# Kernel tuning notes

Measured on AMD Instinct MI355X. Metric: run time of the kernel, lower is better.

## Reference

```python
import jax, jax.numpy as jnp
import numpy as np

K = 20  # neighbors
SLOPE = 0.2  # leaky relu negative slope


def knn_idx(x):
    # x: [B, C, N] -> idx: [B, N, K] indices of K nearest points (incl. self)
    inner = -2.0 * jnp.einsum('bcn,bcm->bnm', x, x)          # [B,N,N]
    xx = jnp.sum(x * x, axis=1)                              # [B,N]
    pairwise = -xx[:, :, None] - inner - xx[:, None, :]      # negative sq dist
    _, idx = jax.lax.top_k(pairwise, K)                      # [B,N,K]
    return idx


def graph_feature(x, idx):
    # x: [B, C, N], idx: [B, N, K] -> [B, N, K, 2C] = cat(neighbor - center, center)
    xt = jnp.transpose(x, (0, 2, 1))                         # [B,N,C]
    nbr = jnp.take_along_axis(xt[:, None, :, :], idx[..., None], axis=2)  # [B,N,K,C]
    ctr = jnp.broadcast_to(xt[:, :, None, :], nbr.shape)     # [B,N,K,C]
    return jnp.concatenate([nbr - ctr, ctr], axis=-1)        # [B,N,K,2C]


def edge_block(x, W):
    # x: [B, C, N]; W: [C_out, 2C] (1x1 conv weight, no bias)
    f = graph_feature(x, knn_idx(x))                         # [B,N,K,2C]
    y = jnp.einsum('bnkc,oc->bonk', f, W)                    # [B,C_out,N,K]
    y = jax.nn.leaky_relu(y, negative_slope=SLOPE)
    return jnp.max(y, axis=-1)                               # [B,C_out,N]


def setup_inputs() -> dict:
    key = jax.random.key(0)
    ks = jax.random.split(key, 6)
    B, N = 8, 2048
    x = jax.random.normal(ks[0], (B, 3, N), dtype=jnp.float32)
    def w(k, o, i):
        return jax.random.normal(k, (o, i), dtype=jnp.float32) * (1.0 / np.sqrt(i))
    W1 = w(ks[1], 64, 6)      # block1: in 3  -> 64
    W2 = w(ks[2], 64, 128)    # block2: in 64 -> 64
    W3 = w(ks[3], 128, 128)   # block3: in 64 -> 128
    W4 = w(ks[4], 256, 256)   # block4: in 128-> 256
    Wg = w(ks[5], 1024, 512)  # global conv1d: 64+64+128+256=512 -> 1024
    return {'x': x, 'W1': W1, 'W2': W2, 'W3': W3, 'W4': W4, 'Wg': Wg}


def reference(x, W1, W2, W3, W4, Wg):
    x1 = edge_block(x, W1)                                   # [B,64,N]
    x2 = edge_block(x1, W2)                                  # [B,64,N]
    x3 = edge_block(x2, W3)                                  # [B,128,N]
    x4 = edge_block(x3, W4)                                  # [B,256,N]
    x_cat = jnp.concatenate([x1, x2, x3, x4], axis=1)        # [B,512,N]
    g = jnp.einsum('bcn,oc->bon', x_cat, Wg)                 # [B,1024,N]
    g = jax.nn.leaky_relu(g, negative_slope=SLOPE)
    return jnp.max(g, axis=-1)                               # [B,1024]
```

## Files before the change

kernel.cpp:

```cpp
#include <hip/hip_runtime.h>
#include <hip/hip_bf16.h>
#include <cfloat>

#define Nn 2048
#define KK 20
#define BB 8
#define SLOPE 0.2f
#define NCH 32

typedef __bf16 bf16x8 __attribute__((ext_vector_type(8)));
typedef float f32x4 __attribute__((ext_vector_type(4)));
typedef unsigned short u16x8 __attribute__((ext_vector_type(8)));

__device__ __forceinline__ unsigned short bfbits(__hip_bfloat16 h) {
    unsigned short us;
    __builtin_memcpy(&us, &h, 2);
    return us;
}


__global__ void wfrag_kernel(const float* __restrict__ W,
                             __hip_bfloat16* __restrict__ Wh, __hip_bfloat16* __restrict__ Wl,
                             int CIN, int Co, int CO2, int KS) {
    int g = blockIdx.x * 256 + threadIdx.x;
    int ng = CO2 * KS * 4;
    if (g >= ng) return;
    int o = g / (KS * 4);
    int c8 = (g - o * (KS * 4)) * 8;
    u16x8 hw, lw;
    #pragma unroll
    for (int t = 0; t < 8; ++t) {
        int c = c8 + t;
        float v = 0.f;
        if (c < CIN) {
            if (o < Co) v = W[(long)o * 2 * CIN + c];
            else        v = W[(long)(o - Co) * 2 * CIN + CIN + c] - W[(long)(o - Co) * 2 * CIN + c];
        }
        __hip_bfloat16 h = __float2bfloat16(v);
        hw[t] = bfbits(h);
        lw[t] = bfbits(__float2bfloat16(v - __bfloat162float(h)));
    }
    long dst = ((long)(o >> 4) * KS + (c8 >> 5)) * 512 + ((o & 15) + 16 * ((c8 >> 3) & 3)) * 8;
    *(u16x8*)(Wh + dst) = hw;
    *(u16x8*)(Wl + dst) = lw;
}

__global__ void tobf16_frag(const float* __restrict__ W, __hip_bfloat16* __restrict__ F) {
    int g = blockIdx.x * 256 + threadIdx.x;
    if (g >= 1024 * 64) return;
    int o = g >> 6, k8 = (g & 63) * 8;
    const float* src = W + (long)o * 512 + k8;
    unsigned short tmp[8];
    #pragma unroll
    for (int t = 0; t < 8; ++t) tmp[t] = bfbits(__float2bfloat16(src[t]));
    long dst = ((long)(o >> 4) * 16 + (k8 >> 5)) * 512 + ((o & 15) + 16 * ((k8 >> 3) & 3)) * 8;
    u16x8 pk;
    #pragma unroll
    for (int t = 0; t < 8; ++t) pk[t] = tmp[t];
    *(u16x8*)(F + dst) = pk;
}

__global__ void split3_kernel(const float* __restrict__ x,
                              __hip_bfloat16* __restrict__ xh,
                              __hip_bfloat16* __restrict__ xl,
                              float* __restrict__ sq) {
    int i = blockIdx.x * 256 + threadIdx.x;
    if (i >= BB * Nn) return;
    const float* xb = x + (long)(i >> 11) * 3 * Nn + (i & 2047);
    float v0 = xb[0], v1 = xb[Nn], v2 = xb[2 * Nn];
    sq[i] = v0 * v0 + v1 * v1 + v2 * v2;
    __hip_bfloat16 h0 = __float2bfloat16(v0), h1 = __float2bfloat16(v1), h2 = __float2bfloat16(v2);
    __hip_bfloat16 l0 = __float2bfloat16(v0 - __bfloat162float(h0));
    __hip_bfloat16 l1 = __float2bfloat16(v1 - __bfloat162float(h1));
    __hip_bfloat16 l2 = __float2bfloat16(v2 - __bfloat162float(h2));
    long base = ((long)(i >> 11) * 128 + ((i & 2047) >> 4)) * 512 + (long)(i & 15) * 8;
    u16x8 z = (u16x8){0, 0, 0, 0, 0, 0, 0, 0};
    u16x8 hw = z, lw = z;
    hw[0] = bfbits(h0); hw[1] = bfbits(h1); hw[2] = bfbits(h2);
    lw[0] = bfbits(l0); lw[1] = bfbits(l1); lw[2] = bfbits(l2);
    *(u16x8*)(xh + base) = hw;
    *(u16x8*)(xl + base) = lw;
    #pragma unroll
    for (int q = 1; q < 4; ++q) {
        *(u16x8*)(xh + base + q * 128) = z;
        *(u16x8*)(xl + base + q * 128) = z;
    }
}

__device__ __forceinline__ unsigned fkey(float f) {
    unsigned u = __float_as_uint(f);
    return u ^ (((unsigned)((int)u >> 31)) | 0x80000000u);
}

template<int C, int NKS>
__global__ void __launch_bounds__(512)
gram_mfma(const __hip_bfloat16* __restrict__ xh, const __hip_bfloat16* __restrict__ xl,
          int ks0, const float* __restrict__ sqv, unsigned* __restrict__ Kbuf) {
    constexpr int KS = C / 32;
    const int tid = threadIdx.x;
    const int w = tid >> 6, lane = tid & 63;
    const int lm = lane & 15, quad = lane >> 4;
    const int nb = blockIdx.x & 7;
    const int mt = (blockIdx.x >> 3) & 15;
    const int b  = blockIdx.x >> 7;
    const int m0 = mt * 128 + (w >> 2) * 64;
    const int j0 = nb * 256 + (w & 3) * 64;

    const long TILE = (long)NKS * 512;
    const __hip_bfloat16* hbase = xh + (long)b * 128 * TILE + (long)ks0 * 512 + lane * 8;
    const __hip_bfloat16* lbase = xl + (long)b * 128 * TILE + (long)ks0 * 512 + lane * 8;
    const __hip_bfloat16* hA = hbase + (long)(m0 >> 4) * TILE;
    const __hip_bfloat16* lA = lbase + (long)(m0 >> 4) * TILE;
    const __hip_bfloat16* hB = hbase + (long)(j0 >> 4) * TILE;
    const __hip_bfloat16* lB = lbase + (long)(j0 >> 4) * TILE;

    f32x4 acc[4][4];
    #pragma unroll
    for (int i = 0; i < 4; ++i)
        #pragma unroll
        for (int j = 0; j < 4; ++j)
            acc[i][j] = (f32x4){0.f, 0.f, 0.f, 0.f};

    #pragma unroll 2
    for (int ks = 0; ks < KS; ++ks) {
        bf16x8 ah[4], alo[4], bh[4], blo[4];
        #pragma unroll
        for (int i = 0; i < 4; ++i) {
            ah[i]  = *(const bf16x8*)(const void*)(hA + (long)i * TILE + ks * 512);
            alo[i] = *(const bf16x8*)(const void*)(lA + (long)i * TILE + ks * 512);
        }
        #pragma unroll
        for (int j = 0; j < 4; ++j) {
            bh[j]  = *(const bf16x8*)(const void*)(hB + (long)j * TILE + ks * 512);
            blo[j] = *(const bf16x8*)(const void*)(lB + (long)j * TILE + ks * 512);
        }
        #pragma unroll
        for (int i = 0; i < 4; ++i)
            #pragma unroll
            for (int j = 0; j < 4; ++j) {
                acc[i][j] = __builtin_amdgcn_mfma_f32_16x16x32_bf16(alo[i], bh[j], acc[i][j], 0, 0, 0);
                acc[i][j] = __builtin_amdgcn_mfma_f32_16x16x32_bf16(ah[i], blo[j], acc[i][j], 0, 0, 0);
                acc[i][j] = __builtin_amdgcn_mfma_f32_16x16x32_bf16(ah[i], bh[j], acc[i][j], 0, 0, 0);
            }
    }

    const float* sqb = sqv + b * Nn;
    float sqj[4];
    #pragma unroll
    for (int j = 0; j < 4; ++j) sqj[j] = sqb[j0 + j * 16 + lm];

    unsigned* Kb = Kbuf + (long)b * Nn * Nn;
    #pragma unroll
    for (int i = 0; i < 4; ++i) {
        #pragma unroll
        for (int r = 0; r < 4; ++r) {
            int m = m0 + i * 16 + quad * 4 + r;
            unsigned* row = Kb + (long)m * Nn;
            #pragma unroll
            for (int j = 0; j < 4; ++j)
                row[j0 + j * 16 + lm] = fkey(fmaf(-2.f, acc[i][j][r], sqj[j]));
        }
    }
}

template<int KS, int NKS_A, int CO2>
__global__ void __launch_bounds__(256)
proj_mfma(const __hip_bfloat16* __restrict__ Ah, const __hip_bfloat16* __restrict__ Al,
          int ks0,
          const __hip_bfloat16* __restrict__ Wh, const __hip_bfloat16* __restrict__ Wl,
          float* __restrict__ Z) {
    constexpr int NWo = (CO2 >= 256) ? 4 : 2;
    constexpr int NWm = 4 / NWo;
    constexpr int MT = 2048 / (64 * NWm);
    const int tid = threadIdx.x;
    const int w = tid >> 6, lane = tid & 63;
    const int lm = lane & 15, quad = lane >> 4;
    const int b  = blockIdx.x & 7;
    const int mt = (blockIdx.x >> 3) % MT;
    const int ot = (blockIdx.x >> 3) / MT;
    const int m0 = mt * 64 * NWm + (w / NWo) * 64;
    const int o0 = ot * 64 * NWo + (w % NWo) * 64;

    const long TA = (long)NKS_A * 512;
    const long TW = (long)KS * 512;
    const __hip_bfloat16* hA = Ah + (long)b * 128 * TA + (long)(m0 >> 4) * TA + (long)ks0 * 512 + lane * 8;
    const __hip_bfloat16* lA = Al + (long)b * 128 * TA + (long)(m0 >> 4) * TA + (long)ks0 * 512 + lane * 8;
    const __hip_bfloat16* hW = Wh + (long)(o0 >> 4) * TW + lane * 8;
    const __hip_bfloat16* lW = Wl + (long)(o0 >> 4) * TW + lane * 8;

    f32x4 acc[4][4];
    #pragma unroll
    for (int i = 0; i < 4; ++i)
        #pragma unroll
        for (int j = 0; j < 4; ++j)
            acc[i][j] = (f32x4){0.f, 0.f, 0.f, 0.f};

    #pragma unroll 2
    for (int ks = 0; ks < KS; ++ks) {
        bf16x8 ah[4], alo[4], bh[4], blo[4];
        #pragma unroll
        for (int i = 0; i < 4; ++i) {
            ah[i]  = *(const bf16x8*)(const void*)(hA + (long)i * TA + ks * 512);
            alo[i] = *(const bf16x8*)(const void*)(lA + (long)i * TA + ks * 512);
        }
        #pragma unroll
        for (int j = 0; j < 4; ++j) {
            bh[j]  = *(const bf16x8*)(const void*)(hW + (long)j * TW + ks * 512);
            blo[j] = *(const bf16x8*)(const void*)(lW + (long)j * TW + ks * 512);
        }
        #pragma unroll
        for (int i = 0; i < 4; ++i)
            #pragma unroll
            for (int j = 0; j < 4; ++j) {
                acc[i][j] = __builtin_amdgcn_mfma_f32_16x16x32_bf16(alo[i], bh[j], acc[i][j], 0, 0, 0);
                acc[i][j] = __builtin_amdgcn_mfma_f32_16x16x32_bf16(ah[i], blo[j], acc[i][j], 0, 0, 0);
                acc[i][j] = __builtin_amdgcn_mfma_f32_16x16x32_bf16(ah[i], bh[j], acc[i][j], 0, 0, 0);
            }
    }

    float* Zb = Z + (long)b * 2048 * CO2;
    #pragma unroll
    for (int i = 0; i < 4; ++i) {
        #pragma unroll
        for (int r = 0; r < 4; ++r) {
            int n = m0 + i * 16 + quad * 4 + r;
            float* row = Zb + (long)n * CO2 + o0;
            #pragma unroll
            for (int j = 0; j < 4; ++j)
                row[j * 16 + lm] = acc[i][j][r];
        }
    }
}

__global__ void __launch_bounds__(512)
select_kernel(const unsigned* __restrict__ Kbuf, int* __restrict__ idx) {
    const int tid = threadIdx.x;
    const int b  = blockIdx.x >> 8;
    const int n0 = (blockIdx.x & 255) * 8;
    const int w = tid >> 6, lane = tid & 63;

    const unsigned* drow = Kbuf + ((long)b * Nn + n0 + w) * Nn;
    int* outp = idx + ((long)b * Nn + n0 + w) * KK;

    unsigned long long lm1 = ~0ull, lm2 = ~0ull;
    #pragma unroll
    for (int jj = 0; jj < 8; ++jj) {
        int j4 = (jj * 64 + lane) * 4;
        uint4 v = *(const uint4*)(drow + j4);
        unsigned long long kk0 = ((unsigned long long)v.x << 32) | (unsigned)(j4 + 0);
        unsigned long long kk1 = ((unsigned long long)v.y << 32) | (unsigned)(j4 + 1);
        unsigned long long kk2 = ((unsigned long long)v.z << 32) | (unsigned)(j4 + 2);
        unsigned long long kk3 = ((unsigned long long)v.w << 32) | (unsigned)(j4 + 3);
        unsigned long long hi;
        hi = kk0 > lm1 ? kk0 : lm1; lm1 = kk0 < lm1 ? kk0 : lm1; lm2 = hi < lm2 ? hi : lm2;
        hi = kk1 > lm1 ? kk1 : lm1; lm1 = kk1 < lm1 ? kk1 : lm1; lm2 = hi < lm2 ? hi : lm2;
        hi = kk2 > lm1 ? kk2 : lm1; lm1 = kk2 < lm1 ? kk2 : lm1; lm2 = hi < lm2 ? hi : lm2;
        hi = kk3 > lm1 ? kk3 : lm1; lm1 = kk3 < lm1 ? kk3 : lm1; lm2 = hi < lm2 ? hi : lm2;
    }

    unsigned T;
    {
        unsigned sa = (unsigned)(lm1 >> 32), sb = (unsigned)(lm2 >> 32);
        #pragma unroll
        for (int size = 2; size <= 128; size <<= 1) {
            #pragma unroll
            for (int str = size >> 1; str >= 2; str >>= 1) {
                const int h = str >> 1;
                const bool asc = (((lane << 1) & size) == 0);
                const bool keepmin = (((lane & h) == 0) == asc);
                unsigned pa = __shfl_xor(sa, h, 64);
                unsigned pb = __shfl_xor(sb, h, 64);
                sa = keepmin ? (sa < pa ? sa : pa) : (sa > pa ? sa : pa);
                sb = keepmin ? (sb < pb ? sb : pb) : (sb > pb ? sb : pb);
            }
            const bool asc = (((lane << 1) & size) == 0);
            unsigned mn = sa < sb ? sa : sb;
            unsigned mx = sa < sb ? sb : sa;
            sa = asc ? mn : mx; sb = asc ? mx : mn;
        }
        T = __shfl(sb, 9, 64);
    }

    unsigned long long c0 = 0, c1 = 0, c2 = 0, c3 = 0, c4 = 0, c5 = 0;
    unsigned cnt = 0;
    #pragma unroll
    for (int jj = 0; jj < 8; ++jj) {
        int j4 = (jj * 64 + lane) * 4;
        uint4 v = *(const uint4*)(drow + j4);
        #pragma unroll
        for (int q = 0; q < 4; ++q) {
            unsigned kq = q == 0 ? v.x : q == 1 ? v.y : q == 2 ? v.z : v.w;
            if (kq <= T) {
                unsigned long long kv = ((unsigned long long)kq << 32) | (unsigned)(j4 + q);
                if (cnt == 0) c0 = kv;
                else if (cnt == 1) c1 = kv;
                else if (cnt == 2) c2 = kv;
                else if (cnt == 3) c3 = kv;
                else if (cnt == 4) c4 = kv;
                else if (cnt == 5) c5 = kv;
                ++cnt;
            }
        }
    }

    unsigned tot = cnt;
    #pragma unroll
    for (int s = 1; s < 64; s <<= 1) tot += __shfl_xor(tot, s, 64);
    unsigned long long anyovf = __ballot(cnt > 6);

    if (anyovf == 0 && tot <= 56) {
        int e = (int)tot - KK;
        for (int rr = 0; rr < e; ++rr) {
            unsigned long long mymax = c0;
            if (c1 > mymax) mymax = c1;
            if (c2 > mymax) mymax = c2;
            if (c3 > mymax) mymax = c3;
            if (c4 > mymax) mymax = c4;
            if (c5 > mymax) mymax = c5;
            unsigned long long wm = mymax;
            #pragma unroll
            for (int s = 1; s < 64; s <<= 1) {
                unsigned long long o = __shfl_xor(wm, s, 64);
                wm = o > wm ? o : wm;
            }
            if (mymax == wm) {
                if (c5 == wm) c5 = 0;
                else if (c4 == wm) c4 = 0;
                else if (c3 == wm) c3 = 0;
                else if (c2 == wm) c2 = 0;
                else if (c1 == wm) c1 = 0;
                else c0 = 0;
            }
        }
        unsigned myc = (c0 != 0) + (c1 != 0) + (c2 != 0) + (c3 != 0) + (c4 != 0) + (c5 != 0);
        unsigned inc = myc;
        #pragma unroll
        for (int off = 1; off < 64; off <<= 1) {
            unsigned t2 = __shfl_up(inc, off, 64);
            if (lane >= off) inc += t2;
        }
        int p = (int)(inc - myc);
        if (c0 != 0) outp[p++] = (int)(unsigned)c0;
        if (c1 != 0) outp[p++] = (int)(unsigned)c1;
        if (c2 != 0) outp[p++] = (int)(unsigned)c2;
        if (c3 != 0) outp[p++] = (int)(unsigned)c3;
        if (c4 != 0) outp[p++] = (int)(unsigned)c4;
        if (c5 != 0) outp[p++] = (int)(unsigned)c5;
        return;
    }

    unsigned exl[KK];
    int ne = 0;
    auto scan2x = [&](unsigned long long& m1, unsigned long long& m2) {
        m1 = ~0ull; m2 = ~0ull;
        for (int jj = 0; jj < 8; ++jj) {
            int j4 = (jj * 64 + lane) * 4;
            uint4 v = *(const uint4*)(drow + j4);
            #pragma unroll
            for (int q = 0; q < 4; ++q) {
                unsigned kq = q == 0 ? v.x : q == 1 ? v.y : q == 2 ? v.z : v.w;
                for (int t = 0; t < ne; ++t)
                    if (exl[t] == (unsigned)(j4 + q)) kq = 0xFFFFFFFFu;
                unsigned long long kv = ((unsigned long long)kq << 32) | (unsigned)(j4 + q);
                unsigned long long hi = kv > m1 ? kv : m1;
                m1 = kv < m1 ? kv : m1;
                m2 = hi < m2 ? hi : m2;
            }
        }
    };

    for (int k = 0; k < KK; ++k) {
        unsigned key = (unsigned)(lm1 >> 32);
        unsigned bk = key;
        #pragma unroll
        for (int s = 1; s < 64; s <<= 1) {
            unsigned ob = __shfl_xor(bk, s, 64);
            bk = ob < bk ? ob : bk;
        }
        unsigned long long winners = __ballot(key == bk);
        int wl = (int)(__ffsll((unsigned long long)winners) - 1);
        int bi = (int)__shfl((unsigned)lm1, wl, 64);
        if (lane == 0) outp[k] = bi;
        if (lane == wl) {
            exl[ne++] = (unsigned)bi;
            if (lm2 != ~0ull) { lm1 = lm2; lm2 = ~0ull; }
            else scan2x(lm1, lm2);
        }
    }
}

template<int CO, bool EMIT>
__global__ void __launch_bounds__(256)
gather_max(const float* __restrict__ Z, const int* __restrict__ idx,
           __hip_bfloat16* __restrict__ xbT, __hip_bfloat16* __restrict__ xbTlo,
           float* __restrict__ sqv, int coff) {
    constexpr int CO2 = 2 * CO;
    constexpr int VEC = CO / 64;
    __shared__ int ji[16][KK];
    const int tid = threadIdx.x;
    const int b  = blockIdx.x & 7;
    const int n0 = (blockIdx.x >> 3) * 16;
    const float* Zb = Z + (long)b * 2048 * CO2;

    for (int t = tid; t < 16 * KK; t += 256) {
        int nn = t / KK, k = t - nn * KK;
        ji[nn][k] = idx[((long)b * Nn + n0 + nn) * KK + k];
    }
    __syncthreads();

    const int w = tid >> 6, lane = tid & 63;
    for (int i = 0; i < 4; ++i) {
        int nl = w * 4 + i, n = n0 + nl;
        float mx[VEC];
        #pragma unroll
        for (int v = 0; v < VEC; ++v) mx[v] = -FLT_MAX;
        for (int k = 0; k < KK; ++k) {
            int m = ji[nl][k];
            const float* zr = Zb + (long)m * CO2 + lane * VEC;
            if constexpr (VEC == 4) {
                float4 zv = *(const float4*)zr;
                mx[0] = fmaxf(mx[0], zv.x); mx[1] = fmaxf(mx[1], zv.y);
                mx[2] = fmaxf(mx[2], zv.z); mx[3] = fmaxf(mx[3], zv.w);
            } else if constexpr (VEC == 2) {
                float2 zv = *(const float2*)zr;
                mx[0] = fmaxf(mx[0], zv.x); mx[1] = fmaxf(mx[1], zv.y);
            } else {
                mx[0] = fmaxf(mx[0], zr[0]);
            }
        }
        const float* zc = Zb + (long)n * CO2 + CO + lane * VEC;
        const int c0 = coff + lane * VEC;
        const long fbase = ((long)b * 128 + (n >> 4)) * 8192
                         + (long)(c0 >> 5) * 512
                         + (long)(((n & 15) + 16 * ((c0 >> 3) & 3)) * 8) + (c0 & 7);
        __hip_bfloat16* xr = xbT + fbase;
        float y[VEC];
        if constexpr (VEC == 4) {
            float4 cv = *(const float4*)zc;
            y[0] = mx[0] + cv.x; y[1] = mx[1] + cv.y; y[2] = mx[2] + cv.z; y[3] = mx[3] + cv.w;
        } else if constexpr (VEC == 2) {
            float2 cv = *(const float2*)zc;
            y[0] = mx[0] + cv.x; y[1] = mx[1] + cv.y;
        } else {
            y[0] = mx[0] + zc[0];
        }
        unsigned short hb[VEC], lb[VEC];
        float s = 0.f;
        #pragma unroll
        for (int v = 0; v < VEC; ++v) {
            y[v] = y[v] > 0.f ? y[v] : SLOPE * y[v];
            __hip_bfloat16 h = __float2bfloat16(y[v]);
            hb[v] = bfbits(h);
            if constexpr (EMIT) {
                lb[v] = bfbits(__float2bfloat16(y[v] - __bfloat162float(h)));
                s += y[v] * y[v];
            }
        }
        if constexpr (VEC == 4) {
            ushort4 pk; pk.x = hb[0]; pk.y = hb[1]; pk.z = hb[2]; pk.w = hb[3];
            *(ushort4*)xr = pk;
        } else if constexpr (VEC == 2) {
            ushort2 pk; pk.x = hb[0]; pk.y = hb[1];
            *(ushort2*)xr = pk;
        } else {
            *(unsigned short*)xr = hb[0];
        }
        if constexpr (EMIT) {
            __hip_bfloat16* lr = xbTlo + fbase;
            if constexpr (VEC == 4) {
                ushort4 pk; pk.x = lb[0]; pk.y = lb[1]; pk.z = lb[2]; pk.w = lb[3];
                *(ushort4*)lr = pk;
            } else if constexpr (VEC == 2) {
                ushort2 pk; pk.x = lb[0]; pk.y = lb[1];
                *(ushort2*)lr = pk;
            } else {
                *(unsigned short*)lr = lb[0];
            }
            #pragma unroll
            for (int off = 1; off < 64; off <<= 1) s += __shfl_xor(s, off, 64);
            if (lane == 0) sqv[b * Nn + n] = s;
        }
    }
}

__global__ void __launch_bounds__(512)
global_mfma(const __hip_bfloat16* __restrict__ Wgf,
            const __hip_bfloat16* __restrict__ xbT,
            float* __restrict__ partial) {
    const int tid = threadIdx.x;
    const int w = tid >> 6, lane = tid & 63;
    const int lm = lane & 15, quad = lane >> 4;
    const int b  = blockIdx.x >> 6;
    const int ot = (blockIdx.x >> 3) & 7;
    const int nb = blockIdx.x & 7;
    const int o0 = ot * 128 + (w >> 2) * 64;
    const int nbw = nb * 256 + (w & 3) * 64;

    const __hip_bfloat16* Af = Wgf + (long)(o0 >> 4) * 8192 + lane * 8;
    const __hip_bfloat16* Bf = xbT + ((long)b * 128 + (nbw >> 4)) * 8192 + lane * 8;

    f32x4 acc[4][4];
    #pragma unroll
    for (int mt = 0; mt < 4; ++mt)
        #pragma unroll
        for (int nt = 0; nt < 4; ++nt)
            acc[mt][nt] = (f32x4){0.f, 0.f, 0.f, 0.f};

    #pragma unroll 2
    for (int ks = 0; ks < 16; ++ks) {
        bf16x8 a[4], bb[4];
        #pragma unroll
        for (int mt = 0; mt < 4; ++mt)
            a[mt] = *(const bf16x8*)(const void*)(Af + (long)mt * 8192 + ks * 512);
        #pragma unroll
        for (int nt = 0; nt < 4; ++nt)
            bb[nt] = *(const bf16x8*)(const void*)(Bf + (long)nt * 8192 + ks * 512);
        #pragma unroll
        for (int mt = 0; mt < 4; ++mt)
            #pragma unroll
            for (int nt = 0; nt < 4; ++nt)
                acc[mt][nt] = __builtin_amdgcn_mfma_f32_16x16x32_bf16(
                    a[mt], bb[nt], acc[mt][nt], 0, 0, 0);
    }

    #pragma unroll
    for (int mt = 0; mt < 4; ++mt) {
        #pragma unroll
        for (int r = 0; r < 4; ++r) {
            float v = fmaxf(fmaxf(acc[mt][0][r], acc[mt][1][r]),
                            fmaxf(acc[mt][2][r], acc[mt][3][r]));
            #pragma unroll
            for (int s = 1; s < 16; s <<= 1)
                v = fmaxf(v, __shfl_xor(v, s, 16));
            if (lm == 0) {
                int o = o0 + mt * 16 + quad * 4 + r;
                partial[((long)b * 1024 + o) * NCH + nb * 4 + (w & 3)] = v;
            }
        }
    }
}

__global__ void gmax_kernel(const float* __restrict__ partial, float* __restrict__ out) {
    int i = blockIdx.x * 256 + threadIdx.x;
    float m = -FLT_MAX;
    #pragma unroll
    for (int j = 0; j < NCH; ++j) m = fmaxf(m, partial[(long)i * NCH + j]);
    out[i] = m > 0.f ? m : SLOPE * m;
}

extern "C" void kernel_launch(void* const* d_in, const int* in_sizes, int n_in,
                              void* d_out, int out_size, void* d_ws, size_t ws_size,
                              hipStream_t stream) {
    const float* x  = (const float*)d_in[0];
    const float* W1 = (const float*)d_in[1];
    const float* W2 = (const float*)d_in[2];
    const float* W3 = (const float*)d_in[3];
    const float* W4 = (const float*)d_in[4];
    const float* Wg = (const float*)d_in[5];
    float* out = (float*)d_out;

    int*   idxb = (int*)d_ws;
    float* part = (float*)(idxb + (long)BB * Nn * KK);
    __hip_bfloat16* Wgb = (__hip_bfloat16*)(part + (long)BB * 1024 * NCH);
    __hip_bfloat16* xbT = Wgb + (long)1024 * 512;
    __hip_bfloat16* xbTlo = xbT + (long)BB * Nn * 512;
    __hip_bfloat16* x1h = xbTlo + (long)BB * Nn * 512;
    __hip_bfloat16* x1l = x1h + (long)BB * Nn * 32;
    float* sq1  = (float*)(x1l + (long)BB * Nn * 32);
    float* sqv  = sq1 + (long)BB * Nn;
    __hip_bfloat16* wf1h = (__hip_bfloat16*)(sqv + (long)BB * Nn);
    __hip_bfloat16* wf1l = wf1h + 8 * 512;
    __hip_bfloat16* wf2h = wf1l + 8 * 512;
    __hip_bfloat16* wf2l = wf2h + 8 * 2 * 512;
    __hip_bfloat16* wf3h = wf2l + 8 * 2 * 512;
    __hip_bfloat16* wf3l = wf3h + 16 * 2 * 512;
    __hip_bfloat16* wf4h = wf3l + 16 * 2 * 512;
    __hip_bfloat16* wf4l = wf4h + 32 * 4 * 512;
    float* Z    = (float*)(wf4l + 32 * 4 * 512);
    unsigned* Kbuf = (unsigned*)Z;

    wfrag_kernel<<<(128 * 4 + 255) / 256, 256, 0, stream>>>(W1, wf1h, wf1l, 3, 64, 128, 1);
    wfrag_kernel<<<(128 * 8 + 255) / 256, 256, 0, stream>>>(W2, wf2h, wf2l, 64, 64, 128, 2);
    wfrag_kernel<<<(256 * 8 + 255) / 256, 256, 0, stream>>>(W3, wf3h, wf3l, 64, 128, 256, 2);
    wfrag_kernel<<<(512 * 16 + 255) / 256, 256, 0, stream>>>(W4, wf4h, wf4l, 128, 256, 512, 4);
    tobf16_frag<<<(1024 * 64 + 255) / 256, 256, 0, stream>>>(Wg, Wgb);
    split3_kernel<<<(BB * Nn) / 256, 256, 0, stream>>>(x, x1h, x1l, sq1);

    const int gram_grid = BB * 16 * 8;
    const int sel_grid  = BB * (Nn / 8);
    const int ep_grid   = (Nn / 16) * BB;

    gram_mfma<32, 1><<<gram_grid, 512, 0, stream>>>(x1h, x1l, 0, sq1, Kbuf);
    select_kernel<<<sel_grid, 512, 0, stream>>>(Kbuf, idxb);
    proj_mfma<1, 1, 128><<<8 * 16, 256, 0, stream>>>(x1h, x1l, 0, wf1h, wf1l, Z);
    gather_max<64, true><<<ep_grid, 256, 0, stream>>>(Z, idxb, xbT, xbTlo, sqv, 0);
    gram_mfma<64, 16><<<gram_grid, 512, 0, stream>>>(xbT, xbTlo, 0, sqv, Kbuf);
    select_kernel<<<sel_grid, 512, 0, stream>>>(Kbuf, idxb);
    proj_mfma<2, 16, 128><<<8 * 16, 256, 0, stream>>>(xbT, xbTlo, 0, wf2h, wf2l, Z);
    gather_max<64, true><<<ep_grid, 256, 0, stream>>>(Z, idxb, xbT, xbTlo, sqv, 64);
    gram_mfma<64, 16><<<gram_grid, 512, 0, stream>>>(xbT, xbTlo, 2, sqv, Kbuf);
    select_kernel<<<sel_grid, 512, 0, stream>>>(Kbuf, idxb);
    proj_mfma<2, 16, 256><<<8 * 32, 256, 0, stream>>>(xbT, xbTlo, 2, wf3h, wf3l, Z);
    gather_max<128, true><<<ep_grid, 256, 0, stream>>>(Z, idxb, xbT, xbTlo, sqv, 128);
    gram_mfma<128, 16><<<gram_grid, 512, 0, stream>>>(xbT, xbTlo, 4, sqv, Kbuf);
    select_kernel<<<sel_grid, 512, 0, stream>>>(Kbuf, idxb);
    proj_mfma<4, 16, 512><<<8 * 32 * 2, 256, 0, stream>>>(xbT, xbTlo, 4, wf4h, wf4l, Z);
    gather_max<256, false><<<ep_grid, 256, 0, stream>>>(Z, idxb, xbT, xbTlo, sqv, 256);

    global_mfma<<<BB * 8 * 8, 512, 0, stream>>>(Wgb, xbT, part);
    gmax_kernel<<<BB * 1024 / 256, 256, 0, stream>>>(part, out);
}
```

Before: 495.3 us.

## Remap block indices for XCD locality and simplify kNN threshold selection

Permutes blockIdx in the gram and global MFMA kernels so that consecutive blocks, which are dispatched round-robin across XCDs, get grouped by batch and tile on the same die. The aim is better L2 reuse of shared operand tiles. The select kernel now takes a single per-lane minimum and runs a 64-wide bitonic sort, using the 20th smallest lane-min as the threshold. This replaces the two-smallest-per-lane tracking, at the cost of a looser threshold and an extra scan to recompute lm1/lm2 before extraction.

```diff
diff --git a/kernel.cpp b/kernel.cpp
--- a/kernel.cpp
+++ b/kernel.cpp
@@ -100,9 +100,10 @@
     const int tid = threadIdx.x;
     const int w = tid >> 6, lane = tid & 63;
     const int lm = lane & 15, quad = lane >> 4;
-    const int nb = blockIdx.x & 7;
-    const int mt = (blockIdx.x >> 3) & 15;
-    const int b  = blockIdx.x >> 7;
+    const int wg = (blockIdx.x & 7) * 128 + (blockIdx.x >> 3);
+    const int nb = wg & 7;
+    const int mt = (wg >> 3) & 15;
+    const int b  = wg >> 7;
     const int m0 = mt * 128 + (w >> 2) * 64;
     const int j0 = nb * 256 + (w & 3) * 64;
 
@@ -242,43 +243,31 @@
     const unsigned* drow = Kbuf + ((long)b * Nn + n0 + w) * Nn;
     int* outp = idx + ((long)b * Nn + n0 + w) * KK;
 
-    unsigned long long lm1 = ~0ull, lm2 = ~0ull;
+    unsigned mn = 0xFFFFFFFFu;
     #pragma unroll
     for (int jj = 0; jj < 8; ++jj) {
         int j4 = (jj * 64 + lane) * 4;
         uint4 v = *(const uint4*)(drow + j4);
-        unsigned long long kk0 = ((unsigned long long)v.x << 32) | (unsigned)(j4 + 0);
-        unsigned long long kk1 = ((unsigned long long)v.y << 32) | (unsigned)(j4 + 1);
-        unsigned long long kk2 = ((unsigned long long)v.z << 32) | (unsigned)(j4 + 2);
-        unsigned long long kk3 = ((unsigned long long)v.w << 32) | (unsigned)(j4 + 3);
-        unsigned long long hi;
-        hi = kk0 > lm1 ? kk0 : lm1; lm1 = kk0 < lm1 ? kk0 : lm1; lm2 = hi < lm2 ? hi : lm2;
-        hi = kk1 > lm1 ? kk1 : lm1; lm1 = kk1 < lm1 ? kk1 : lm1; lm2 = hi < lm2 ? hi : lm2;
-        hi = kk2 > lm1 ? kk2 : lm1; lm1 = kk2 < lm1 ? kk2 : lm1; lm2 = hi < lm2 ? hi : lm2;
-        hi = kk3 > lm1 ? kk3 : lm1; lm1 = kk3 < lm1 ? kk3 : lm1; lm2 = hi < lm2 ? hi : lm2;
+        unsigned m01 = v.x < v.y ? v.x : v.y;
+        unsigned m23 = v.z < v.w ? v.z : v.w;
+        unsigned m = m01 < m23 ? m01 : m23;
+        mn = m < mn ? m : mn;
     }
 
     unsigned T;
     {
-        unsigned sa = (unsigned)(lm1 >> 32), sb = (unsigned)(lm2 >> 32);
-        #pragma unroll
-        for (int size = 2; size <= 128; size <<= 1) {
-            #pragma unroll
-            for (int str = size >> 1; str >= 2; str >>= 1) {
-                const int h = str >> 1;
-                const bool asc = (((lane << 1) & size) == 0);
-                const bool keepmin = (((lane & h) == 0) == asc);
-                unsigned pa = __shfl_xor(sa, h, 64);
-                unsigned pb = __shfl_xor(sb, h, 64);
+        unsigned sa = mn;
+        #pragma unroll
+        for (int size = 2; size <= 64; size <<= 1) {
+            #pragma unroll
+            for (int str = size >> 1; str >= 1; str >>= 1) {
+                const bool asc = ((lane & size) == 0);
+                const bool keepmin = (((lane & str) == 0) == asc);
+                unsigned pa = __shfl_xor(sa, str, 64);
                 sa = keepmin ? (sa < pa ? sa : pa) : (sa > pa ? sa : pa);
-                sb = keepmin ? (sb < pb ? sb : pb) : (sb > pb ? sb : pb);
-            }
-            const bool asc = (((lane << 1) & size) == 0);
-            unsigned mn = sa < sb ? sa : sb;
-            unsigned mx = sa < sb ? sb : sa;
-            sa = asc ? mn : mx; sb = asc ? mx : mn;
-        }
-        T = __shfl(sb, 9, 64);
+            }
+        }
+        T = __shfl(sa, 19, 64);
     }
 
     unsigned long long c0 = 0, c1 = 0, c2 = 0, c3 = 0, c4 = 0, c5 = 0;
@@ -369,6 +358,8 @@
         }
     };
 
+    unsigned long long lm1, lm2;
+    scan2x(lm1, lm2);
     for (int k = 0; k < KK; ++k) {
         unsigned key = (unsigned)(lm1 >> 32);
         unsigned bk = key;
@@ -490,9 +481,10 @@
     const int tid = threadIdx.x;
     const int w = tid >> 6, lane = tid & 63;
     const int lm = lane & 15, quad = lane >> 4;
-    const int b  = blockIdx.x >> 6;
-    const int ot = (blockIdx.x >> 3) & 7;
-    const int nb = blockIdx.x & 7;
+    const int wg = (blockIdx.x & 7) * 64 + (blockIdx.x >> 3);
+    const int b  = wg >> 6;
+    const int ot = (wg >> 3) & 7;
+    const int nb = wg & 7;
     const int o0 = ot * 128 + (w >> 2) * 64;
     const int nbw = nb * 256 + (w & 3) * 64;
 
```

After: 468.8 us. -5.4%, faster.
